# Kernel tuning notes

Measured on AMD Instinct MI355X. Metric: run time of the kernel, lower is better.

## Reference

```python
import jax, jax.numpy as jnp
import numpy as np

N, E, IN_C, HID, HEADS, OUT_C, NG = 50000, 800000, 300, 64, 2, 2, 256


def _lin(key, fan_in, fan_out):
    k1, k2 = jax.random.split(key)
    lim = 1.0 / np.sqrt(fan_in)
    W = jax.random.uniform(k1, (fan_in, fan_out), jnp.float32, -lim, lim)
    b = jax.random.uniform(k2, (fan_out,), jnp.float32, -lim, lim)
    return W, b


def setup_inputs() -> dict:
    key = jax.random.key(0)
    ks = jax.random.split(key, 16)
    x = jax.random.normal(ks[0], (N, IN_C), jnp.float32)
    edge_index = jax.random.randint(ks[1], (2, E), 0, N, jnp.int64)
    batch = jnp.sort(jax.random.randint(ks[2], (N,), 0, NG, jnp.int64))
    d = {"x": x, "edge_index": edge_index, "batch": batch}
    d["syn_W"], d["syn_b"] = _lin(ks[3], IN_C, HID)
    d["ant_W"], d["ant_b"] = _lin(ks[4], IN_C, HID)
    d["fus_W"], d["fus_b"] = _lin(ks[5], 2 * HID, HID * HEADS)
    # conv1: in=HID*HEADS, out=HID, heads=HEADS (concat)
    d["c1_Wq"], d["c1_bq"] = _lin(ks[6], HID * HEADS, HEADS * HID)
    d["c1_Wk"], d["c1_bk"] = _lin(ks[7], HID * HEADS, HEADS * HID)
    d["c1_Wv"], d["c1_bv"] = _lin(ks[8], HID * HEADS, HEADS * HID)
    d["c1_Ws"], d["c1_bs"] = _lin(ks[9], HID * HEADS, HEADS * HID)
    # conv2: in=HID*HEADS, out=HID, heads=1
    d["c2_Wq"], d["c2_bq"] = _lin(ks[10], HID * HEADS, HID)
    d["c2_Wk"], d["c2_bk"] = _lin(ks[11], HID * HEADS, HID)
    d["c2_Wv"], d["c2_bv"] = _lin(ks[12], HID * HEADS, HID)
    d["c2_Ws"], d["c2_bs"] = _lin(ks[13], HID * HEADS, HID)
    d["l1_W"], d["l1_b"] = _lin(ks[14], HID, HID)
    d["l2_W"], d["l2_b"] = _lin(ks[15], HID, OUT_C)
    return d


def transformer_conv(x, src, dst, Wq, bq, Wk, bk, Wv, bv, Ws, bs, heads, d_head):
    # PyG TransformerConv (concat=True, root_weight=True, eval mode)
    q = (x @ Wq + bq).reshape(-1, heads, d_head)  # [N,H,D]
    k = (x @ Wk + bk).reshape(-1, heads, d_head)
    v = (x @ Wv + bv).reshape(-1, heads, d_head)
    qi = q[dst]  # [E,H,D]
    kj = k[src]
    vj = v[src]
    alpha = jnp.einsum("ehd,ehd->eh", qi, kj) / jnp.sqrt(jnp.float32(d_head))
    amax = jax.ops.segment_max(alpha, dst, num_segments=x.shape[0])
    ealpha = jnp.exp(alpha - amax[dst])
    denom = jax.ops.segment_sum(ealpha, dst, num_segments=x.shape[0])
    alpha = ealpha / (denom[dst] + 1e-16)
    out = jax.ops.segment_sum(alpha[..., None] * vj, dst, num_segments=x.shape[0])
    out = out.reshape(x.shape[0], heads * d_head)
    return out + x @ Ws + bs


def reference(x, edge_index, batch, syn_W, syn_b, ant_W, ant_b, fus_W, fus_b,
              c1_Wq, c1_bq, c1_Wk, c1_bk, c1_Wv, c1_bv, c1_Ws, c1_bs,
              c2_Wq, c2_bq, c2_Wk, c2_bk, c2_Wv, c2_bv, c2_Ws, c2_bs,
              l1_W, l1_b, l2_W, l2_b):
    src, dst = edge_index[0], edge_index[1]
    x_syn = jax.nn.relu(x @ syn_W + syn_b)
    x_ant = jax.nn.relu(x @ ant_W + ant_b)
    x_fused = jnp.concatenate([x_syn, x_ant], axis=1) @ fus_W + fus_b  # [N, HID*HEADS]
    h = transformer_conv(x_fused, src, dst, c1_Wq, c1_bq, c1_Wk, c1_bk,
                         c1_Wv, c1_bv, c1_Ws, c1_bs, HEADS, HID)
    h = jax.nn.relu(h)
    h = transformer_conv(h, src, dst, c2_Wq, c2_bq, c2_Wk, c2_bk,
                         c2_Wv, c2_bv, c2_Ws, c2_bs, 1, HID)
    # global mean pool over graphs
    sums = jax.ops.segment_sum(h, batch, num_segments=NG)
    cnts = jax.ops.segment_sum(jnp.ones((h.shape[0], 1), h.dtype), batch, num_segments=NG)
    pooled = sums / jnp.maximum(cnts, 1.0)
    out = jax.nn.relu(pooled @ l1_W + l1_b)
    return out @ l2_W + l2_b
```

## Files before the change

### kernel.cpp

```cpp
#include <hip/hip_runtime.h>
#include <math.h>

#define NNODES 50000
#define NEDGES 800000
#define INC    300
#define NGRAPH 256

typedef __attribute__((ext_vector_type(8))) short bf16x8;
typedef __attribute__((ext_vector_type(4))) short bf16x4;
typedef __attribute__((ext_vector_type(4))) float f32x4;

#define L2E8 0.180336880f
#define SW(row, k) ((k) ^ (((row) & 7) << 3))
#define EB 3125
#define FRONT_BLOCKS 782
#define FF_GRID (FRONT_BLOCKS + EB)

__device__ __forceinline__ unsigned short f2bf(float f) {
    unsigned u = __float_as_uint(f);
    u += 0x7fffu + ((u >> 16) & 1u);
    return (unsigned short)(u >> 16);
}
__device__ __forceinline__ float bf2f(unsigned short h) {
    return __uint_as_float(((unsigned)h) << 16);
}

struct WTArgs {
    const float* w[11];
    unsigned short* o[11];
    int K[11];
    int N[11];
    int mode[11];
    int roff[11];
    const float* syn_b; const float* ant_b;
    const float* c1q; const float* c1k; const float* c1v; const float* c1s;
    const float* c2q; const float* c2k; const float* c2v; const float* c2s;
    float* enc_b;
    float* c1_b;
    float* c2_b;
};

__global__ void k_setup(WTArgs a, const int* __restrict__ dstv, int* __restrict__ deg) {
    int bx = blockIdx.x;
    if (bx < EB) {
        int e = bx * 256 + threadIdx.x;
        if (e < NEDGES) atomicAdd(&deg[dstv[e]], 1);
        return;
    }
    bx -= EB;
    int which = bx / 75;
    int sub = bx - which * 75;
    if (which == 11) {
        if (sub != 0) return;
        int t = threadIdx.x;
        for (int u = t; u < 896; u += 256) {
            if (u < 512) {
                int s = u >> 7, r = u & 127;
                const float* p = (s == 0) ? a.c1q : (s == 1) ? a.c1k : (s == 2) ? a.c1v : a.c1s;
                a.c1_b[u] = p[r];
            } else if (u < 768) {
                int v = u - 512;
                int s = v >> 6, r = v & 63;
                const float* p = (s == 0) ? a.c2q : (s == 1) ? a.c2k : (s == 2) ? a.c2v : a.c2s;
                a.c2_b[v] = p[r];
            } else {
                int v = u - 768;
                a.enc_b[v] = (v < 64) ? a.syn_b[v] : a.ant_b[v - 64];
            }
        }
        return;
    }
    int i = sub * 256 + threadIdx.x;
    int K = a.K[which], N = a.N[which];
    if (i >= K * N) return;
    int k = i / N, n = i - k * N;
    unsigned short v = f2bf(a.w[which][i]);
    size_t dst;
    int m = a.mode[which];
    if (m == 1) {
        int row = a.roff[which] + n;
        dst = (size_t)(k >> 6) * 8192 + row * 64 + SW(row, k & 63);
    } else if (m == 2) {
        dst = (size_t)n * 128 + SW(n, k);
    } else {
        dst = (size_t)n * K + k;
    }
    a.o[which][dst] = v;
}

__global__ void k_scan1(const int* __restrict__ deg, int* __restrict__ ex,
                        int* __restrict__ bsum, int n) {
    __shared__ int tmp[256];
    int i = blockIdx.x * 256 + threadIdx.x;
    int v = (i < n) ? deg[i] : 0;
    tmp[threadIdx.x] = v;
    __syncthreads();
    for (int off = 1; off < 256; off <<= 1) {
        int t = (threadIdx.x >= off) ? tmp[threadIdx.x - off] : 0;
        __syncthreads();
        tmp[threadIdx.x] += t;
        __syncthreads();
    }
    if (i < n) ex[i] = tmp[threadIdx.x] - v;
    if (threadIdx.x == 255) bsum[blockIdx.x] = tmp[255];
}

__global__ void k_scan2(int* __restrict__ bsum, int nb) {
    __shared__ int tmp[256];
    int v = (threadIdx.x < nb) ? bsum[threadIdx.x] : 0;
    tmp[threadIdx.x] = v;
    __syncthreads();
    for (int off = 1; off < 256; off <<= 1) {
        int t = (threadIdx.x >= off) ? tmp[threadIdx.x - off] : 0;
        __syncthreads();
        tmp[threadIdx.x] += t;
        __syncthreads();
    }
    if (threadIdx.x < nb) bsum[threadIdx.x] = tmp[threadIdx.x] - v;
}

__global__ void k_scan3(int* __restrict__ rp, const int* __restrict__ bsum,
                        int* __restrict__ cursor, int n, int E) {
    int i = blockIdx.x * 256 + threadIdx.x;
    if (i < n) {
        int r = rp[i] + bsum[blockIdx.x];
        rp[i] = r;
        cursor[i] = r;
    }
    if (i == 0) rp[n] = E;
}

__global__ __launch_bounds__(256) void k_front_fill(
    const float* __restrict__ x,
    const unsigned short* __restrict__ enc_img, const float* __restrict__ enc_b,
    const unsigned short* __restrict__ fus_img, const float* __restrict__ fus_b,
    const unsigned short* __restrict__ c1_img, const float* __restrict__ c1_b,
    unsigned short* __restrict__ qkvs1, int M,
    const int* __restrict__ src, const int* __restrict__ dstv,
    int* __restrict__ cursor, int* __restrict__ esrc)
{
    const int b = blockIdx.x;
    const int q = b / 5, r5 = b - q * 5;
    const int tid = threadIdx.x;
    if (!(r5 == 0 && q < FRONT_BLOCKS)) {
        int nf = (b + 4) / 5;
        if (nf > FRONT_BLOCKS) nf = FRONT_BLOCKS;
        int e = (b - nf) * 256 + tid;
        if (e < NEDGES) {
            int d = dstv[e];
            int p = atomicAdd(&cursor[d], 1);
            esrc[p] = src[e];
        }
        return;
    }
    __shared__ __align__(16) char pool[49152];
    short* bufI = (short*)pool;
    short* Bt   = (short*)(pool + 16384);
    short* At   = (short*)(pool + 32768);
    const int bm = q * 64;
    const int tr = tid >> 4;
    const int tc = (tid & 15) * 4;
    const int l  = tid & 63;
    const int wv = tid >> 6;
    const int fr = l & 15;
    const int fg = l >> 4;

    f32x4 acc1[8];
    #pragma unroll
    for (int j = 0; j < 8; ++j) acc1[j] = (f32x4){0.f, 0.f, 0.f, 0.f};

    for (int ph = 0; ph < 5; ++ph) {
        int k0 = ph * 64;
        {
            bf16x8* d = (bf16x8*)Bt;
            const bf16x8* s = (const bf16x8*)(enc_img + ph * 8192);
            #pragma unroll
            for (int i = 0; i < 4; ++i) d[tid + i * 256] = s[tid + i * 256];
        }
        #pragma unroll
        for (int p = 0; p < 4; ++p) {
            int row = p * 16 + tr;
            int grow = bm + row;
            int k = k0 + tc;
            float x0 = 0.f, x1 = 0.f, x2 = 0.f, x3 = 0.f;
            if (grow < M) {
                if (k + 4 <= INC) {
                    float4 a4 = *reinterpret_cast<const float4*>(x + (size_t)grow * INC + k);
                    x0 = a4.x; x1 = a4.y; x2 = a4.z; x3 = a4.w;
                } else {
                    if (k + 0 < INC) x0 = x[(size_t)grow * INC + k + 0];
                    if (k + 1 < INC) x1 = x[(size_t)grow * INC + k + 1];
                    if (k + 2 < INC) x2 = x[(size_t)grow * INC + k + 2];
                    if (k + 3 < INC) x3 = x[(size_t)grow * INC + k + 3];
                }
            }
            bf16x4 s4 = { (short)f2bf(x0), (short)f2bf(x1), (short)f2bf(x2), (short)f2bf(x3) };
            *reinterpret_cast<bf16x4*>(At + row * 64 + SW(row, tc)) = s4;
        }
        __syncthreads();
        #pragma unroll
        for (int ks = 0; ks < 2; ++ks) {
            int kk = ks * 32 + fg * 8;
            int ar = wv * 16 + fr;
            bf16x8 a0 = *reinterpret_cast<const bf16x8*>(At + ar * 64 + SW(ar, kk));
            #pragma unroll
            for (int nj = 0; nj < 8; ++nj) {
                int br = nj * 16 + fr;
                bf16x8 bfr = *reinterpret_cast<const bf16x8*>(Bt + br * 64 + SW(br, kk));
                acc1[nj] = __builtin_amdgcn_mfma_f32_16x16x32_bf16(a0, bfr, acc1[nj], 0, 0, 0);
            }
        }
        __syncthreads();
    }
    #pragma unroll
    for (int nj = 0; nj < 8; ++nj) {
        int col = nj * 16 + fr;
        float bv = enc_b[col];
        #pragma unroll
        for (int r = 0; r < 4; ++r) {
            int row = wv * 16 + fg * 4 + r;
            float val = fmaxf(acc1[nj][r] + bv, 0.f);
            bufI[row * 128 + SW(row, col)] = (short)f2bf(val);
        }
    }
    __syncthreads();

    bf16x8 af[4];
    {
        int ar = wv * 16 + fr;
        #pragma unroll
        for (int t = 0; t < 4; ++t)
            af[t] = *reinterpret_cast<const bf16x8*>(bufI + ar * 128 + SW(ar, fg * 8 + t * 32));
    }
    __syncthreads();
    {
        bf16x8* d = (bf16x8*)Bt;
        const bf16x8* s = (const bf16x8*)fus_img;
        #pragma unroll
        for (int i = 0; i < 8; ++i) d[tid + i * 256] = s[tid + i * 256];
    }
    __syncthreads();

    f32x4 acc2[8];
    #pragma unroll
    for (int j = 0; j < 8; ++j) acc2[j] = (f32x4){0.f, 0.f, 0.f, 0.f};
    #pragma unroll
    for (int t = 0; t < 4; ++t) {
        int k = t * 32 + fg * 8;
        #pragma unroll
        for (int nj = 0; nj < 8; ++nj) {
            int br = nj * 16 + fr;
            bf16x8 bfr = *reinterpret_cast<const bf16x8*>(Bt + br * 128 + SW(br, k));
            acc2[nj] = __builtin_amdgcn_mfma_f32_16x16x32_bf16(af[t], bfr, acc2[nj], 0, 0, 0);
        }
    }
    __syncthreads();
    #pragma unroll
    for (int nj = 0; nj < 8; ++nj) {
        int col = nj * 16 + fr;
        float bv = fus_b[col];
        #pragma unroll
        for (int r = 0; r < 4; ++r) {
            int row = wv * 16 + fg * 4 + r;
            bufI[row * 128 + SW(row, col)] = (short)f2bf(acc2[nj][r] + bv);
        }
    }
    __syncthreads();

    bf16x8 af2[4];
    {
        int ar = wv * 16 + fr;
        #pragma unroll
        for (int t = 0; t < 4; ++t)
            af2[t] = *reinterpret_cast<const bf16x8*>(bufI + ar * 128 + SW(ar, fg * 8 + t * 32));
    }

    #pragma unroll
    for (int cc = 0; cc < 4; ++cc) {
        __syncthreads();
        {
            bf16x8* d = (bf16x8*)Bt;
            const bf16x8* s = (const bf16x8*)(c1_img + cc * 16384);
            #pragma unroll
            for (int i = 0; i < 8; ++i) d[tid + i * 256] = s[tid + i * 256];
        }
        __syncthreads();
        f32x4 acc3[8];
        #pragma unroll
        for (int j = 0; j < 8; ++j) acc3[j] = (f32x4){0.f, 0.f, 0.f, 0.f};
        #pragma unroll
        for (int t = 0; t < 4; ++t) {
            int k = t * 32 + fg * 8;
            #pragma unroll
            for (int nj = 0; nj < 8; ++nj) {
                int br = nj * 16 + fr;
                bf16x8 bfr = *reinterpret_cast<const bf16x8*>(Bt + br * 128 + SW(br, k));
                acc3[nj] = __builtin_amdgcn_mfma_f32_16x16x32_bf16(af2[t], bfr, acc3[nj], 0, 0, 0);
            }
        }
        #pragma unroll
        for (int nj = 0; nj < 8; ++nj) {
            int col = cc * 128 + nj * 16 + fr;
            float bv = c1_b[col];
            #pragma unroll
            for (int r = 0; r < 4; ++r) {
                int gr = bm + wv * 16 + fg * 4 + r;
                if (gr < M)
                    qkvs1[(size_t)gr * 512 + col] = f2bf(acc3[nj][r] + bv);
            }
        }
    }
}

#define BM 128

template<int BNT>
__global__ __launch_bounds__(256) void gemm_mfma(
    const unsigned short* __restrict__ A, int lda, int M, int K,
    const unsigned short* __restrict__ Wt,
    const float* __restrict__ bias,
    unsigned short* __restrict__ C, int ldc)
{
    __shared__ __align__(16) short As[BM * 64];
    __shared__ __align__(16) short Bs[BNT * 64];
    const int tid = threadIdx.x;
    const int bm = blockIdx.x * BM;
    const int bn = blockIdx.y * BNT;
    const int tr = tid >> 4;
    const int tc = (tid & 15) * 4;
    const int l  = tid & 63;
    const int wv = tid >> 6;
    const int fr = l & 15;
    const int fg = l >> 4;

    f32x4 acc[2][BNT / 16];
    #pragma unroll
    for (int i = 0; i < 2; ++i)
        #pragma unroll
        for (int j = 0; j < BNT / 16; ++j) acc[i][j] = (f32x4){0.f, 0.f, 0.f, 0.f};

    for (int k0 = 0; k0 < K; k0 += 64) {
        #pragma unroll
        for (int p = 0; p < 8; ++p) {
            int row = p * 16 + tr;
            int grow = bm + row;
            int k = k0 + tc;
            bf16x4 s4 = (bf16x4){0, 0, 0, 0};
            if (grow < M) s4 = *reinterpret_cast<const bf16x4*>(A + (size_t)grow * lda + k);
            *reinterpret_cast<bf16x4*>(As + row * 64 + SW(row, tc)) = s4;
        }
        #pragma unroll
        for (int p = 0; p < BNT / 16; ++p) {
            int n = p * 16 + tr;
            *reinterpret_cast<bf16x4*>(Bs + n * 64 + SW(n, tc)) =
                *reinterpret_cast<const bf16x4*>(Wt + (size_t)(bn + n) * K + k0 + tc);
        }
        __syncthreads();
        #pragma unroll
        for (int ks = 0; ks < 2; ++ks) {
            int kk = ks * 32 + fg * 8;
            int ar0 = wv * 32 + fr, ar1 = wv * 32 + 16 + fr;
            bf16x8 a0 = *reinterpret_cast<const bf16x8*>(As + ar0 * 64 + SW(ar0, kk));
            bf16x8 a1 = *reinterpret_cast<const bf16x8*>(As + ar1 * 64 + SW(ar1, kk));
            #pragma unroll
            for (int nj = 0; nj < BNT / 16; ++nj) {
                int br = nj * 16 + fr;
                bf16x8 b = *reinterpret_cast<const bf16x8*>(Bs + br * 64 + SW(br, kk));
                acc[0][nj] = __builtin_amdgcn_mfma_f32_16x16x32_bf16(a0, b, acc[0][nj], 0, 0, 0);
                acc[1][nj] = __builtin_amdgcn_mfma_f32_16x16x32_bf16(a1, b, acc[1][nj], 0, 0, 0);
            }
        }
        __syncthreads();
    }
    #pragma unroll
    for (int mi = 0; mi < 2; ++mi) {
        int row0 = bm + wv * 32 + mi * 16 + fg * 4;
        #pragma unroll
        for (int nj = 0; nj < BNT / 16; ++nj) {
            int col = bn + nj * 16 + fr;
            float bv = bias[col];
            #pragma unroll
            for (int r = 0; r < 4; ++r) {
                int gr = row0 + r;
                if (gr >= M) continue;
                C[(size_t)gr * ldc + col] = f2bf(acc[mi][nj][r] + bv);
            }
        }
    }
}

__global__ __launch_bounds__(256) void attn_h2(
    const unsigned short* __restrict__ qkvs,
    const int* __restrict__ rowptr, const int* __restrict__ esrc,
    unsigned short* __restrict__ outp, int N)
{
    int wid = (blockIdx.x * blockDim.x + threadIdx.x) >> 6;
    int l = threadIdx.x & 63;
    if (wid >= N) return;
    const int sl = l & 15;
    const int g  = l >> 4;
    const unsigned short* bi = qkvs + (size_t)wid * 512;
    float q[8];
    {
        bf16x8 qv = *reinterpret_cast<const bf16x8*>(bi + 8 * sl);
        #pragma unroll
        for (int i = 0; i < 8; ++i) q[i] = bf2f((unsigned short)qv[i]) * L2E8;
    }
    float s = 0.f;
    float acc[8] = {0.f, 0.f, 0.f, 0.f, 0.f, 0.f, 0.f, 0.f};
    const int beg = rowptr[wid], end = rowptr[wid + 1];
    const int iters = (end - beg + 3) >> 2;
    int e = beg + g;
    bool va0 = e < end;
    int j0 = va0 ? esrc[e] : wid;
    const unsigned short* pp0 = qkvs + (size_t)j0 * 512 + 8 * sl;
    bf16x8 ka = *reinterpret_cast<const bf16x8*>(pp0 + 128);
    bf16x8 vva = *reinterpret_cast<const bf16x8*>(pp0 + 256);
    bool va1 = (e + 4) < end;
    int j1 = va1 ? esrc[e + 4] : wid;
    const unsigned short* pp1 = qkvs + (size_t)j1 * 512 + 8 * sl;
    bf16x8 kb = *reinterpret_cast<const bf16x8*>(pp1 + 128);
    bf16x8 vvb = *reinterpret_cast<const bf16x8*>(pp1 + 256);
    for (int it = 0; it < iters; ++it) {
        bf16x8 kc = ka, vc = vva;
        bool vd = va0;
        ka = kb; vva = vvb; va0 = va1;
        va1 = (e + 8) < end;
        int j2 = va1 ? esrc[e + 8] : wid;
        const unsigned short* p2 = qkvs + (size_t)j2 * 512 + 8 * sl;
        kb = *reinterpret_cast<const bf16x8*>(p2 + 128);
        vvb = *reinterpret_cast<const bf16x8*>(p2 + 256);
        e += 4;
        float p = 0.f;
        #pragma unroll
        for (int i = 0; i < 8; ++i) p += q[i] * bf2f((unsigned short)kc[i]);
        p += __shfl_xor(p, 1, 64);
        p += __shfl_xor(p, 2, 64);
        p += __shfl_xor(p, 4, 64);
        float w = vd ? __builtin_amdgcn_exp2f(p) : 0.f;
        s += w;
        #pragma unroll
        for (int i = 0; i < 8; ++i) acc[i] += w * bf2f((unsigned short)vc[i]);
    }
    #pragma unroll
    for (int mask = 16; mask <= 32; mask <<= 1) {
        s += __shfl_xor(s, mask, 64);
        #pragma unroll
        for (int i = 0; i < 8; ++i) acc[i] += __shfl_xor(acc[i], mask, 64);
    }
    if (g == 0) {
        float inv = 1.f / (s + 1e-16f);
        bf16x8 sv = *reinterpret_cast<const bf16x8*>(bi + 384 + 8 * sl);
        bf16x8 o;
        #pragma unroll
        for (int i = 0; i < 8; ++i) {
            float r = fmaxf(acc[i] * inv + bf2f((unsigned short)sv[i]), 0.f);
            o[i] = (short)f2bf(r);
        }
        *reinterpret_cast<bf16x8*>(outp + (size_t)wid * 128 + 8 * sl) = o;
    }
}

__global__ __launch_bounds__(256) void attn_h1(
    const unsigned short* __restrict__ qkvs,
    const int* __restrict__ rowptr, const int* __restrict__ esrc,
    float* __restrict__ outp, int N)
{
    int wid = (blockIdx.x * blockDim.x + threadIdx.x) >> 6;
    int l = threadIdx.x & 63;
    if (wid >= N) return;
    const int sl = l & 7;
    const int g  = l >> 3;
    const unsigned short* bi = qkvs + (size_t)wid * 256;
    float q[8];
    {
        bf16x8 qv = *reinterpret_cast<const bf16x8*>(bi + 8 * sl);
        #pragma unroll
        for (int i = 0; i < 8; ++i) q[i] = bf2f((unsigned short)qv[i]) * L2E8;
    }
    float s = 0.f;
    float acc[8] = {0.f, 0.f, 0.f, 0.f, 0.f, 0.f, 0.f, 0.f};
    const int beg = rowptr[wid], end = rowptr[wid + 1];
    const int iters = (end - beg + 7) >> 3;
    int e = beg + g;
    bool va0 = e < end;
    int j0 = va0 ? esrc[e] : wid;
    const unsigned short* pp0 = qkvs + (size_t)j0 * 256 + 8 * sl;
    bf16x8 ka = *reinterpret_cast<const bf16x8*>(pp0 + 64);
    bf16x8 vva = *reinterpret_cast<const bf16x8*>(pp0 + 128);
    bool va1 = (e + 8) < end;
    int j1 = va1 ? esrc[e + 8] : wid;
    const unsigned short* pp1 = qkvs + (size_t)j1 * 256 + 8 * sl;
    bf16x8 kb = *reinterpret_cast<const bf16x8*>(pp1 + 64);
    bf16x8 vvb = *reinterpret_cast<const bf16x8*>(pp1 + 128);
    for (int it = 0; it < iters; ++it) {
        bf16x8 kc = ka, vc = vva;
        bool vd = va0;
        ka = kb; vva = vvb; va0 = va1;
        va1 = (e + 16) < end;
        int j2 = va1 ? esrc[e + 16] : wid;
        const unsigned short* p2 = qkvs + (size_t)j2 * 256 + 8 * sl;
        kb = *reinterpret_cast<const bf16x8*>(p2 + 64);
        vvb = *reinterpret_cast<const bf16x8*>(p2 + 128);
        e += 8;
        float p = 0.f;
        #pragma unroll
        for (int i = 0; i < 8; ++i) p += q[i] * bf2f((unsigned short)kc[i]);
        p += __shfl_xor(p, 1, 64);
        p += __shfl_xor(p, 2, 64);
        p += __shfl_xor(p, 4, 64);
        float w = vd ? __builtin_amdgcn_exp2f(p) : 0.f;
        s += w;
        #pragma unroll
        for (int i = 0; i < 8; ++i) acc[i] += w * bf2f((unsigned short)vc[i]);
    }
    #pragma unroll
    for (int mask = 8; mask <= 32; mask <<= 1) {
        s += __shfl_xor(s, mask, 64);
        #pragma unroll
        for (int i = 0; i < 8; ++i) acc[i] += __shfl_xor(acc[i], mask, 64);
    }
    if (g == 0) {
        float inv = 1.f / (s + 1e-16f);
        float r[8];
        #pragma unroll
        for (int i = 0; i < 8; ++i)
            r[i] = acc[i] * inv + bf2f(bi[192 + 8 * sl + i]);
        float* op = outp + (size_t)wid * 64 + 8 * sl;
        *reinterpret_cast<float4*>(op)     = make_float4(r[0], r[1], r[2], r[3]);
        *reinterpret_cast<float4*>(op + 4) = make_float4(r[4], r[5], r[6], r[7]);
    }
}

__device__ __forceinline__ int lbound(const int* __restrict__ a, int n, int key) {
    int lo = 0, hi = n;
    while (lo < hi) {
        int mid = (lo + hi) >> 1;
        if (a[mid] < key) lo = mid + 1; else hi = mid;
    }
    return lo;
}

__global__ void pool_head(const float* __restrict__ h, const int* __restrict__ batch,
                          const float* __restrict__ l1W, const float* __restrict__ l1b,
                          const float* __restrict__ l2W, const float* __restrict__ l2b,
                          float* __restrict__ out) {
    __shared__ float red[4][64];
    int g = blockIdx.x;
    int l = threadIdx.x & 63;
    int w = threadIdx.x >> 6;
    int lo = lbound(batch, NNODES, g);
    int hi = lbound(batch, NNODES, g + 1);
    float s = 0.f;
    for (int i = lo + w; i < hi; i += 4) s += h[(size_t)i * 64 + l];
    red[w][l] = s;
    __syncthreads();
    if (w == 0) {
        float t = red[0][l] + red[1][l] + red[2][l] + red[3][l];
        float cnt = (float)((hi - lo) > 1 ? (hi - lo) : 1);
        float p = t / cnt;
        float hsum = l1b[l];
        #pragma unroll
        for (int kk = 0; kk < 64; ++kk) {
            float pk = __shfl(p, kk, 64);
            hsum += pk * l1W[kk * 64 + l];
        }
        float hr = fmaxf(hsum, 0.f);
        float o0 = hr * l2W[l * 2 + 0];
        float o1 = hr * l2W[l * 2 + 1];
        #pragma unroll
        for (int off = 32; off > 0; off >>= 1) {
            o0 += __shfl_xor(o0, off, 64);
            o1 += __shfl_xor(o1, off, 64);
        }
        if (l == 0) {
            out[g * 2 + 0] = o0 + l2b[0];
            out[g * 2 + 1] = o1 + l2b[1];
        }
    }
}

extern "C" void kernel_launch(void* const* d_in, const int* in_sizes, int n_in,
                              void* d_out, int out_size, void* d_ws, size_t ws_size,
                              hipStream_t stream) {
    const float* x      = (const float*)d_in[0];
    const int*   ei     = (const int*)d_in[1];
    const int*   batch  = (const int*)d_in[2];
    const float* syn_W  = (const float*)d_in[3];  const float* syn_b = (const float*)d_in[4];
    const float* ant_W  = (const float*)d_in[5];  const float* ant_b = (const float*)d_in[6];
    const float* fus_W  = (const float*)d_in[7];  const float* fus_b = (const float*)d_in[8];
    const float* c1_Wq  = (const float*)d_in[9];  const float* c1_bq = (const float*)d_in[10];
    const float* c1_Wk  = (const float*)d_in[11]; const float* c1_bk = (const float*)d_in[12];
    const float* c1_Wv  = (const float*)d_in[13]; const float* c1_bv = (const float*)d_in[14];
    const float* c1_Ws  = (const float*)d_in[15]; const float* c1_bs = (const float*)d_in[16];
    const float* c2_Wq  = (const float*)d_in[17]; const float* c2_bq = (const float*)d_in[18];
    const float* c2_Wk  = (const float*)d_in[19]; const float* c2_bk = (const float*)d_in[20];
    const float* c2_Wv  = (const float*)d_in[21]; const float* c2_bv = (const float*)d_in[22];
    const float* c2_Ws  = (const float*)d_in[23]; const float* c2_bs = (const float*)d_in[24];
    const float* l1_W   = (const float*)d_in[25]; const float* l1_b  = (const float*)d_in[26];
    const float* l2_W   = (const float*)d_in[27]; const float* l2_b  = (const float*)d_in[28];
    const int* src = ei;
    const int* dst = ei + NEDGES;
    float* out = (float*)d_out;

    char* ws = (char*)d_ws;
    size_t off = 0;
    auto alloc = [&](size_t bytes) -> char* {
        char* p = ws + off;
        off += (bytes + 255) & ~((size_t)255);
        return p;
    };

    unsigned short* H     = (unsigned short*)alloc((size_t)NNODES * 128 * 2);
    unsigned short* H2b   = (unsigned short*)alloc((size_t)NNODES * 128 * 2);
    unsigned short* qkvs1 = (unsigned short*)alloc((size_t)NNODES * 512 * 2);
    unsigned short* qkvs2 = (unsigned short*)alloc((size_t)NNODES * 256 * 2);
    unsigned short* enc_img = (unsigned short*)alloc((size_t)5 * 8192 * 2);
    unsigned short* fus_img = (unsigned short*)alloc((size_t)16384 * 2);
    unsigned short* c1_img  = (unsigned short*)alloc((size_t)4 * 16384 * 2);
    unsigned short* c2w_t   = (unsigned short*)alloc((size_t)256 * 128 * 2);
    float* enc_b = (float*)alloc(128 * 4);
    float* c1_b  = (float*)alloc(512 * 4);
    float* c2_b  = (float*)alloc(256 * 4);
    int*   deg    = (int*)alloc((NNODES + 1) * 4);
    int*   cursor = (int*)alloc((NNODES + 1) * 4);
    int*   rowptr = (int*)alloc((NNODES + 1) * 4);
    int*   bsum   = (int*)alloc(256 * 4);
    int*   esrc   = (int*)alloc((size_t)NEDGES * 4);

    const int NB = (NNODES + 255) / 256;
    dim3 t256(256);

    WTArgs wa;
    wa.w[0] = syn_W;  wa.o[0] = enc_img;  wa.K[0] = 300; wa.N[0] = 64;  wa.mode[0] = 1; wa.roff[0] = 0;
    wa.w[1] = ant_W;  wa.o[1] = enc_img;  wa.K[1] = 300; wa.N[1] = 64;  wa.mode[1] = 1; wa.roff[1] = 64;
    wa.w[2] = fus_W;  wa.o[2] = fus_img;  wa.K[2] = 128; wa.N[2] = 128; wa.mode[2] = 2; wa.roff[2] = 0;
    wa.w[3] = c1_Wq;  wa.o[3] = c1_img + 0 * 16384; wa.K[3] = 128; wa.N[3] = 128; wa.mode[3] = 2; wa.roff[3] = 0;
    wa.w[4] = c1_Wk;  wa.o[4] = c1_img + 1 * 16384; wa.K[4] = 128; wa.N[4] = 128; wa.mode[4] = 2; wa.roff[4] = 0;
    wa.w[5] = c1_Wv;  wa.o[5] = c1_img + 2 * 16384; wa.K[5] = 128; wa.N[5] = 128; wa.mode[5] = 2; wa.roff[5] = 0;
    wa.w[6] = c1_Ws;  wa.o[6] = c1_img + 3 * 16384; wa.K[6] = 128; wa.N[6] = 128; wa.mode[6] = 2; wa.roff[6] = 0;
    wa.w[7] = c2_Wq;  wa.o[7] = c2w_t + 0 * 64 * 128;  wa.K[7] = 128; wa.N[7] = 64; wa.mode[7] = 0; wa.roff[7] = 0;
    wa.w[8] = c2_Wk;  wa.o[8] = c2w_t + 1 * 64 * 128;  wa.K[8] = 128; wa.N[8] = 64; wa.mode[8] = 0; wa.roff[8] = 0;
    wa.w[9] = c2_Wv;  wa.o[9] = c2w_t + 2 * 64 * 128;  wa.K[9] = 128; wa.N[9] = 64; wa.mode[9] = 0; wa.roff[9] = 0;
    wa.w[10] = c2_Ws; wa.o[10] = c2w_t + 3 * 64 * 128; wa.K[10] = 128; wa.N[10] = 64; wa.mode[10] = 0; wa.roff[10] = 0;
    wa.syn_b = syn_b; wa.ant_b = ant_b;
    wa.c1q = c1_bq; wa.c1k = c1_bk; wa.c1v = c1_bv; wa.c1s = c1_bs;
    wa.c2q = c2_bq; wa.c2k = c2_bk; wa.c2v = c2_bv; wa.c2s = c2_bs;
    wa.enc_b = enc_b; wa.c1_b = c1_b; wa.c2_b = c2_b;

    hipMemsetAsync(deg, 0, (NNODES + 1) * sizeof(int), stream);
    hipMemsetAsync(enc_img, 0, (size_t)5 * 8192 * 2, stream);
    k_setup<<<EB + 900, t256, 0, stream>>>(wa, dst, deg);

    k_scan1<<<NB, t256, 0, stream>>>(deg, rowptr, bsum, NNODES);
    k_scan2<<<1, t256, 0, stream>>>(bsum, NB);
    k_scan3<<<NB, t256, 0, stream>>>(rowptr, bsum, cursor, NNODES, NEDGES);

    k_front_fill<<<FF_GRID, t256, 0, stream>>>(
        x, enc_img, enc_b, fus_img, fus_b, c1_img, c1_b, qkvs1, NNODES,
        src, dst, cursor, esrc);

    attn_h2<<<(NNODES * 64 + 255) / 256, t256, 0, stream>>>(qkvs1, rowptr, esrc, H, NNODES);

    gemm_mfma<128><<<dim3((NNODES + BM - 1) / BM, 2), t256, 0, stream>>>(
        H, 128, NNODES, 128, c2w_t, c2_b, qkvs2, 256);

    float* H2 = (float*)H2b;
    attn_h1<<<(NNODES * 64 + 255) / 256, t256, 0, stream>>>(qkvs2, rowptr, esrc, H2, NNODES);

    pool_head<<<NGRAPH, t256, 0, stream>>>(H2, batch, l1_W, l1_b, l2_W, l2_b, out);
}
```

Baseline: 286.3 us.

## Prepack x into MFMA fragment layout, double-buffer encoder weights, coalesce GEMM stores

The setup kernel now converts x to bf16 and writes it in a fragment-ordered layout, so the front GEMM loads A operands straight into registers with no shared-memory staging. Encoder weight tiles are double-buffered through registers so each phase overlaps the next load, which removes one barrier per phase. Output tiles in both the front kernel and gemm_mfma are staged through shared memory and written as 16-byte rows instead of scattered 2-byte stores. The cost is an extra pass over x, a new 30MB buffer that must be zeroed by a memset, and more register pressure from holding ten A fragments per thread.

```diff
diff --git a/kernel.cpp b/kernel.cpp
--- a/kernel.cpp
+++ b/kernel.cpp
@@ -13,6 +13,7 @@
 #define L2E8 0.180336880f
 #define SW(row, k) ((k) ^ (((row) & 7) << 3))
 #define EB 3125
+#define XPB 14649
 #define FRONT_BLOCKS 782
 #define FF_GRID (FRONT_BLOCKS + EB)
 
@@ -40,7 +41,8 @@
     float* c2_b;
 };
 
-__global__ void k_setup(WTArgs a, const int* __restrict__ dstv, int* __restrict__ deg) {
+__global__ void k_setup(WTArgs a, const int* __restrict__ dstv, int* __restrict__ deg,
+                        const float* __restrict__ x, unsigned short* __restrict__ xp) {
     int bx = blockIdx.x;
     if (bx < EB) {
         int e = bx * 256 + threadIdx.x;
@@ -48,6 +50,22 @@
         return;
     }
     bx -= EB;
+    if (bx < XPB) {
+        int i = bx * 256 + threadIdx.x;
+        if (i < NNODES * 75) {
+            int row = i / 75;
+            int col = (i - row * 75) * 4;
+            float4 v = *reinterpret_cast<const float4*>(x + (size_t)row * INC + col);
+            int q = row >> 6, wv = (row >> 4) & 3, fr = row & 15;
+            int t = col >> 5, fg = (col >> 3) & 3, j = col & 7;
+            size_t base = ((((size_t)(q * 4 + wv) * 10 + t) * 64) + fg * 16 + fr) * 8 + j;
+            ushort4 o;
+            o.x = f2bf(v.x); o.y = f2bf(v.y); o.z = f2bf(v.z); o.w = f2bf(v.w);
+            *reinterpret_cast<ushort4*>(xp + base) = o;
+        }
+        return;
+    }
+    bx -= XPB;
     int which = bx / 75;
     int sub = bx - which * 75;
     if (which == 11) {
@@ -131,7 +149,7 @@
 }
 
 __global__ __launch_bounds__(256) void k_front_fill(
-    const float* __restrict__ x,
+    const unsigned short* __restrict__ xp,
     const unsigned short* __restrict__ enc_img, const float* __restrict__ enc_b,
     const unsigned short* __restrict__ fus_img, const float* __restrict__ fus_b,
     const unsigned short* __restrict__ c1_img, const float* __restrict__ c1_b,
@@ -153,62 +171,60 @@
         }
         return;
     }
-    __shared__ __align__(16) char pool[49152];
-    short* bufI = (short*)pool;
-    short* Bt   = (short*)(pool + 16384);
-    short* At   = (short*)(pool + 32768);
+    __shared__ __align__(16) short P[24576];
+    short* bufI = P;
+    short* B0   = P + 8192;
+    short* B1   = P + 16384;
+    short* Bt   = P + 8192;
     const int bm = q * 64;
-    const int tr = tid >> 4;
-    const int tc = (tid & 15) * 4;
     const int l  = tid & 63;
     const int wv = tid >> 6;
     const int fr = l & 15;
     const int fg = l >> 4;
 
+    bf16x8 aP[10];
+    {
+        const unsigned short* xpb = xp + (((size_t)(q * 4 + wv) * 10) * 64 + l) * 8;
+        #pragma unroll
+        for (int t = 0; t < 10; ++t)
+            aP[t] = *reinterpret_cast<const bf16x8*>(xpb + (size_t)t * 512);
+    }
+
     f32x4 acc1[8];
     #pragma unroll
     for (int j = 0; j < 8; ++j) acc1[j] = (f32x4){0.f, 0.f, 0.f, 0.f};
 
+    {
+        bf16x8* d = (bf16x8*)B0;
+        const bf16x8* s = (const bf16x8*)enc_img;
+        #pragma unroll
+        for (int i = 0; i < 4; ++i) d[tid + i * 256] = s[tid + i * 256];
+    }
+    __syncthreads();
     for (int ph = 0; ph < 5; ++ph) {
-        int k0 = ph * 64;
-        {
-            bf16x8* d = (bf16x8*)Bt;
-            const bf16x8* s = (const bf16x8*)(enc_img + ph * 8192);
+        short* cur = (ph & 1) ? B1 : B0;
+        short* nxt = (ph & 1) ? B0 : B1;
+        bf16x8 tmp[4];
+        if (ph < 4) {
+            const bf16x8* s = (const bf16x8*)(enc_img + (ph + 1) * 8192);
             #pragma unroll
-            for (int i = 0; i < 4; ++i) d[tid + i * 256] = s[tid + i * 256];
-        }
-        #pragma unroll
-        for (int p = 0; p < 4; ++p) {
-            int row = p * 16 + tr;
-            int grow = bm + row;
-            int k = k0 + tc;
-            float x0 = 0.f, x1 = 0.f, x2 = 0.f, x3 = 0.f;
-            if (grow < M) {
-                if (k + 4 <= INC) {
-                    float4 a4 = *reinterpret_cast<const float4*>(x + (size_t)grow * INC + k);
-                    x0 = a4.x; x1 = a4.y; x2 = a4.z; x3 = a4.w;
-                } else {
-                    if (k + 0 < INC) x0 = x[(size_t)grow * INC + k + 0];
-                    if (k + 1 < INC) x1 = x[(size_t)grow * INC + k + 1];
-                    if (k + 2 < INC) x2 = x[(size_t)grow * INC + k + 2];
-                    if (k + 3 < INC) x3 = x[(size_t)grow * INC + k + 3];
-                }
-            }
-            bf16x4 s4 = { (short)f2bf(x0), (short)f2bf(x1), (short)f2bf(x2), (short)f2bf(x3) };
-            *reinterpret_cast<bf16x4*>(At + row * 64 + SW(row, tc)) = s4;
-        }
-        __syncthreads();
+            for (int i = 0; i < 4; ++i) tmp[i] = s[tid + i * 256];
+        }
         #pragma unroll
         for (int ks = 0; ks < 2; ++ks) {
             int kk = ks * 32 + fg * 8;
-            int ar = wv * 16 + fr;
-            bf16x8 a0 = *reinterpret_cast<const bf16x8*>(At + ar * 64 + SW(ar, kk));
+            int t = ph * 2 + ks;
             #pragma unroll
             for (int nj = 0; nj < 8; ++nj) {
                 int br = nj * 16 + fr;
-                bf16x8 bfr = *reinterpret_cast<const bf16x8*>(Bt + br * 64 + SW(br, kk));
-                acc1[nj] = __builtin_amdgcn_mfma_f32_16x16x32_bf16(a0, bfr, acc1[nj], 0, 0, 0);
+                bf16x8 bfr = *reinterpret_cast<const bf16x8*>(cur + br * 64 + SW(br, kk));
+                acc1[nj] = __builtin_amdgcn_mfma_f32_16x16x32_bf16(aP[t], bfr, acc1[nj], 0, 0, 0);
             }
+        }
+        if (ph < 4) {
+            bf16x8* d = (bf16x8*)nxt;
+            #pragma unroll
+            for (int i = 0; i < 4; ++i) d[tid + i * 256] = tmp[i];
         }
         __syncthreads();
     }
@@ -300,14 +316,24 @@
         }
         #pragma unroll
         for (int nj = 0; nj < 8; ++nj) {
-            int col = cc * 128 + nj * 16 + fr;
-            float bv = c1_b[col];
+            int col = nj * 16 + fr;
+            float bv = c1_b[cc * 128 + col];
             #pragma unroll
             for (int r = 0; r < 4; ++r) {
-                int gr = bm + wv * 16 + fg * 4 + r;
-                if (gr < M)
-                    qkvs1[(size_t)gr * 512 + col] = f2bf(acc3[nj][r] + bv);
+                int row = wv * 16 + fg * 4 + r;
+                bufI[row * 128 + col] = (short)f2bf(acc3[nj][r] + bv);
             }
+        }
+        __syncthreads();
+        #pragma unroll
+        for (int i = 0; i < 4; ++i) {
+            int p = tid + i * 256;
+            int row = p >> 4;
+            int c8 = (p & 15) * 8;
+            int gr = bm + row;
+            if (gr < M)
+                *reinterpret_cast<bf16x8*>(qkvs1 + (size_t)gr * 512 + cc * 128 + c8) =
+                    *reinterpret_cast<const bf16x8*>(bufI + row * 128 + c8);
         }
     }
 }
@@ -374,18 +400,28 @@
     }
     #pragma unroll
     for (int mi = 0; mi < 2; ++mi) {
-        int row0 = bm + wv * 32 + mi * 16 + fg * 4;
         #pragma unroll
         for (int nj = 0; nj < BNT / 16; ++nj) {
-            int col = bn + nj * 16 + fr;
-            float bv = bias[col];
+            int col = nj * 16 + fr;
+            float bv = bias[bn + col];
             #pragma unroll
             for (int r = 0; r < 4; ++r) {
-                int gr = row0 + r;
-                if (gr >= M) continue;
-                C[(size_t)gr * ldc + col] = f2bf(acc[mi][nj][r] + bv);
+                int lr = wv * 16 + fg * 4 + r;
+                As[lr * BNT + col] = (short)f2bf(acc[mi][nj][r] + bv);
             }
         }
+        __syncthreads();
+        #pragma unroll
+        for (int i = 0; i < 4; ++i) {
+            int p = tid + i * 256;
+            int lr = p >> 4;
+            int c8 = (p & 15) * 8;
+            int grow = bm + (lr >> 4) * 32 + mi * 16 + (lr & 15);
+            if (grow < M)
+                *reinterpret_cast<bf16x8*>(C + (size_t)grow * ldc + bn + c8) =
+                    *reinterpret_cast<const bf16x8*>(As + lr * BNT + c8);
+        }
+        __syncthreads();
     }
 }
 
@@ -615,6 +651,7 @@
     unsigned short* H2b   = (unsigned short*)alloc((size_t)NNODES * 128 * 2);
     unsigned short* qkvs1 = (unsigned short*)alloc((size_t)NNODES * 512 * 2);
     unsigned short* qkvs2 = (unsigned short*)alloc((size_t)NNODES * 256 * 2);
+    unsigned short* xp    = (unsigned short*)alloc((size_t)FRONT_BLOCKS * 4 * 10 * 512 * 2);
     unsigned short* enc_img = (unsigned short*)alloc((size_t)5 * 8192 * 2);
     unsigned short* fus_img = (unsigned short*)alloc((size_t)16384 * 2);
     unsigned short* c1_img  = (unsigned short*)alloc((size_t)4 * 16384 * 2);
@@ -649,15 +686,16 @@
     wa.enc_b = enc_b; wa.c1_b = c1_b; wa.c2_b = c2_b;
 
     hipMemsetAsync(deg, 0, (NNODES + 1) * sizeof(int), stream);
+    hipMemsetAsync(xp, 0, (size_t)FRONT_BLOCKS * 4 * 10 * 512 * 2, stream);
     hipMemsetAsync(enc_img, 0, (size_t)5 * 8192 * 2, stream);
-    k_setup<<<EB + 900, t256, 0, stream>>>(wa, dst, deg);
+    k_setup<<<EB + XPB + 900, t256, 0, stream>>>(wa, dst, deg, x, xp);
 
     k_scan1<<<NB, t256, 0, stream>>>(deg, rowptr, bsum, NNODES);
     k_scan2<<<1, t256, 0, stream>>>(bsum, NB);
     k_scan3<<<NB, t256, 0, stream>>>(rowptr, bsum, cursor, NNODES, NEDGES);
 
     k_front_fill<<<FF_GRID, t256, 0, stream>>>(
-        x, enc_img, enc_b, fus_img, fus_b, c1_img, c1_b, qkvs1, NNODES,
+        xp, enc_img, enc_b, fus_img, fus_b, c1_img, c1_b, qkvs1, NNODES,
         src, dst, cursor, esrc);
 
     attn_h2<<<(NNODES * 64 + 255) / 256, t256, 0, stream>>>(qkvs1, rowptr, esrc, H, NNODES);
```

Measured after the change: 265.2 us. 7.4% less time.
